# Kernel tuning notes

Measured on AMD Instinct MI355X. Metric: run time of the kernel, lower is better.

The kernel has to match this reference:

```python
import jax, jax.numpy as jnp
import numpy as np

B, T, P = 32, 400, 10000  # batch, num_tf, num_peak


def setup_inputs() -> dict:
    key = jax.random.key(0)
    k_x, k_w, k_fc = jax.random.split(key, 3)
    x = jax.random.normal(k_x, (B, T, P), dtype=jnp.float32)
    W = jax.random.normal(k_w, (T, P), dtype=jnp.float32)
    fc1_w = jax.random.normal(k_fc, (1, T * P), dtype=jnp.float32) * 0.01
    fc1_b = jnp.zeros((1,), dtype=jnp.float32)
    return {"x": x, "W": W, "fc1_w": fc1_w, "fc1_b": fc1_b}


def reference(x, W, fc1_w, fc1_b):
    # x: [B, T, P]; W: [T, P]; fc1_w: [1, T*P]; fc1_b: [1]
    # out_b = sum_{t,p} x[b,t,p] * |W[t,p]| * fc1_w[0, t*P+p] + fc1_b
    xw = x * jnp.abs(W)[None, :, :]            # [B, T, P]
    flat = xw.reshape(x.shape[0], -1)          # [B, T*P]
    out = flat @ fc1_w.T + fc1_b               # [B, 1]
    return out
```

## Files before the change

kernel.cpp:

```cpp
#include <hip/hip_runtime.h>

#define BATCH 32
#define NELEM 4000000
#define N4 (NELEM / 4)
#define BLK 256
#define BPG 8
#define GROUPS (BATCH / BPG)
#define NBLK 512

typedef float f4 __attribute__((ext_vector_type(4)));

__global__ __launch_bounds__(BLK)
void stage1_kernel(const f4* __restrict__ x,
                   const f4* __restrict__ W,
                   const f4* __restrict__ F,
                   float* __restrict__ partials) {
    const int g  = blockIdx.y;
    const int bx = blockIdx.x;
    const f4* __restrict__ xg = x + (size_t)g * BPG * N4;

    float acc[BPG];
    #pragma unroll
    for (int r = 0; r < BPG; ++r) acc[r] = 0.0f;

    const int stride = NBLK * BLK;
    for (int i = bx * BLK + threadIdx.x; i < N4; i += stride) {
        f4 wv = W[i];
        f4 fv = F[i];
        f4 s;
        s.x = fabsf(wv.x) * fv.x;
        s.y = fabsf(wv.y) * fv.y;
        s.z = fabsf(wv.z) * fv.z;
        s.w = fabsf(wv.w) * fv.w;
        const f4* __restrict__ xp = xg + i;
        #pragma unroll
        for (int r = 0; r < BPG; ++r) {
            f4 xv = __builtin_nontemporal_load(xp + (size_t)r * N4);
            acc[r] += xv.x * s.x + xv.y * s.y + xv.z * s.z + xv.w * s.w;
        }
    }

    #pragma unroll
    for (int r = 0; r < BPG; ++r) {
        #pragma unroll
        for (int off = 32; off > 0; off >>= 1)
            acc[r] += __shfl_down(acc[r], off, 64);
    }

    __shared__ float lds[BLK / 64][BPG];
    const int lane = threadIdx.x & 63;
    const int wv   = threadIdx.x >> 6;
    if (lane == 0) {
        #pragma unroll
        for (int r = 0; r < BPG; ++r) lds[wv][r] = acc[r];
    }
    __syncthreads();

    if (threadIdx.x < BPG) {
        const int r = threadIdx.x;
        float t = lds[0][r] + lds[1][r] + lds[2][r] + lds[3][r];
        partials[(size_t)(g * BPG + r) * NBLK + bx] = t;
    }
}

__global__ __launch_bounds__(64)
void stage2_kernel(const float* __restrict__ partials,
                   const float* __restrict__ fc1_b,
                   float* __restrict__ out) {
    const int b    = blockIdx.x;
    const int lane = threadIdx.x;
    float t = 0.0f;
    #pragma unroll
    for (int k = lane; k < NBLK; k += 64) t += partials[(size_t)b * NBLK + k];
    #pragma unroll
    for (int off = 32; off > 0; off >>= 1) t += __shfl_down(t, off, 64);
    if (lane == 0) out[b] = t + fc1_b[0];
}

extern "C" void kernel_launch(void* const* d_in, const int* in_sizes, int n_in,
                              void* d_out, int out_size, void* d_ws, size_t ws_size,
                              hipStream_t stream) {
    const float* x     = (const float*)d_in[0];
    const float* W     = (const float*)d_in[1];
    const float* fc1_w = (const float*)d_in[2];
    const float* fc1_b = (const float*)d_in[3];
    float* out      = (float*)d_out;
    float* partials = (float*)d_ws;

    dim3 grid(NBLK, GROUPS);
    stage1_kernel<<<grid, BLK, 0, stream>>>(
        (const f4*)x, (const f4*)W, (const f4*)fc1_w, partials);
    stage2_kernel<<<BATCH, 64, 0, stream>>>(partials, fc1_b, out);
}
```

Measured before the change: 652.4 us.

## Cache |W|*fc1_w chunk in LDS and loop all batches per block

Each block now computes the scaled weight vector |W|*F for its contiguous chunk once, stores it in LDS, and then streams x for all 32 batch rows over that chunk. This drops the 4x redundant reading of W and F across batch groups. In exchange the grid shrinks to 512 blocks with a large LDS footprint (about 32 KB per block), so occupancy and memory-level parallelism drop. Per-batch reductions go through wave shuffles, and the partials buffer grows to one entry per wave.

Result: slower. 713.0 us (+9.3%).

```diff
diff --git a/kernel.cpp b/kernel.cpp
--- a/kernel.cpp
+++ b/kernel.cpp
@@ -4,9 +4,10 @@
 #define NELEM 4000000
 #define N4 (NELEM / 4)
 #define BLK 256
-#define BPG 8
-#define GROUPS (BATCH / BPG)
 #define NBLK 512
+#define CHUNK ((N4 + NBLK - 1) / NBLK)
+#define WPB (BLK / 64)
+#define PSTRIDE (NBLK * WPB)
 
 typedef float f4 __attribute__((ext_vector_type(4)));
 
@@ -15,51 +16,46 @@
                    const f4* __restrict__ W,
                    const f4* __restrict__ F,
                    float* __restrict__ partials) {
-    const int g  = blockIdx.y;
+    __shared__ f4 s_lds[CHUNK];
     const int bx = blockIdx.x;
-    const f4* __restrict__ xg = x + (size_t)g * BPG * N4;
+    const int t  = threadIdx.x;
+    const int i0 = bx * CHUNK;
+    const int len = (i0 + CHUNK <= N4) ? CHUNK : (N4 - i0);
 
-    float acc[BPG];
-    #pragma unroll
-    for (int r = 0; r < BPG; ++r) acc[r] = 0.0f;
-
-    const int stride = NBLK * BLK;
-    for (int i = bx * BLK + threadIdx.x; i < N4; i += stride) {
-        f4 wv = W[i];
-        f4 fv = F[i];
+    for (int i = t; i < len; i += BLK) {
+        f4 wv = W[i0 + i];
+        f4 fv = F[i0 + i];
         f4 s;
         s.x = fabsf(wv.x) * fv.x;
         s.y = fabsf(wv.y) * fv.y;
         s.z = fabsf(wv.z) * fv.z;
         s.w = fabsf(wv.w) * fv.w;
-        const f4* __restrict__ xp = xg + i;
-        #pragma unroll
-        for (int r = 0; r < BPG; ++r) {
-            f4 xv = __builtin_nontemporal_load(xp + (size_t)r * N4);
-            acc[r] += xv.x * s.x + xv.y * s.y + xv.z * s.z + xv.w * s.w;
-        }
-    }
-
-    #pragma unroll
-    for (int r = 0; r < BPG; ++r) {
-        #pragma unroll
-        for (int off = 32; off > 0; off >>= 1)
-            acc[r] += __shfl_down(acc[r], off, 64);
-    }
-
-    __shared__ float lds[BLK / 64][BPG];
-    const int lane = threadIdx.x & 63;
-    const int wv   = threadIdx.x >> 6;
-    if (lane == 0) {
-        #pragma unroll
-        for (int r = 0; r < BPG; ++r) lds[wv][r] = acc[r];
+        s_lds[i] = s;
     }
     __syncthreads();
 
-    if (threadIdx.x < BPG) {
-        const int r = threadIdx.x;
-        float t = lds[0][r] + lds[1][r] + lds[2][r] + lds[3][r];
-        partials[(size_t)(g * BPG + r) * NBLK + bx] = t;
+    const int lane = t & 63;
+    const int wid  = t >> 6;
+
+    for (int r = 0; r < BATCH; ++r) {
+        const f4* __restrict__ xr = x + (size_t)r * N4 + i0;
+        float acc[4] = {0.f, 0.f, 0.f, 0.f};
+        #pragma unroll
+        for (int k = 0; k < 8; ++k) {
+            const int i = k * BLK + t;
+            if (i < len) {
+                f4 xv = __builtin_nontemporal_load(xr + i);
+                f4 sv = s_lds[i];
+                acc[k & 3] += xv.x * sv.x + xv.y * sv.y
+                            + xv.z * sv.z + xv.w * sv.w;
+            }
+        }
+        float a = (acc[0] + acc[1]) + (acc[2] + acc[3]);
+        #pragma unroll
+        for (int off = 32; off > 0; off >>= 1)
+            a += __shfl_down(a, off, 64);
+        if (lane == 0)
+            partials[(size_t)r * PSTRIDE + bx * WPB + wid] = a;
     }
 }
 
@@ -70,8 +66,7 @@
     const int b    = blockIdx.x;
     const int lane = threadIdx.x;
     float t = 0.0f;
-    #pragma unroll
-    for (int k = lane; k < NBLK; k += 64) t += partials[(size_t)b * NBLK + k];
+    for (int k = lane; k < PSTRIDE; k += 64) t += partials[(size_t)b * PSTRIDE + k];
     #pragma unroll
     for (int off = 32; off > 0; off >>= 1) t += __shfl_down(t, off, 64);
     if (lane == 0) out[b] = t + fc1_b[0];
@@ -87,8 +82,7 @@
     float* out      = (float*)d_out;
     float* partials = (float*)d_ws;
 
-    dim3 grid(NBLK, GROUPS);
-    stage1_kernel<<<grid, BLK, 0, stream>>>(
+    stage1_kernel<<<NBLK, BLK, 0, stream>>>(
         (const f4*)x, (const f4*)W, (const f4*)fc1_w, partials);
     stage2_kernel<<<BATCH, 64, 0, stream>>>(partials, fc1_b, out);
 }
```
